# Kernel optimization log

Measured on AMD Instinct MI355X. Metric: run time of the kernel, lower is better.

The kernel has to match this reference:

```python
import math
import jax, jax.numpy as jnp
import numpy as np

EMBED_DIM = 1024
NUM_HEADS = 16
HEAD_DIM = EMBED_DIM // NUM_HEADS
B, S = 4, 2048


def setup_inputs() -> dict:
    key = jax.random.key(0)
    ks = jax.random.split(key, 12)
    sc = 1.0 / math.sqrt(EMBED_DIM)
    inp = {
        "query": jax.random.normal(ks[0], (B, S, EMBED_DIM), jnp.float32),
        "key": jax.random.normal(ks[1], (B, S, EMBED_DIM), jnp.float32),
        "value": jax.random.normal(ks[2], (B, S, EMBED_DIM), jnp.float32),
        # causal mask: True = masked (upper triangle above diagonal)
        "attn_mask": jnp.triu(jnp.ones((S, S), jnp.bool_), k=1),
        "q_w": jax.random.normal(ks[3], (EMBED_DIM, EMBED_DIM), jnp.float32) * sc,
        "q_b": jax.random.normal(ks[4], (EMBED_DIM,), jnp.float32) * sc,
        "k_w": jax.random.normal(ks[5], (EMBED_DIM, EMBED_DIM), jnp.float32) * sc,
        "k_b": jax.random.normal(ks[6], (EMBED_DIM,), jnp.float32) * sc,
        "v_w": jax.random.normal(ks[7], (EMBED_DIM, EMBED_DIM), jnp.float32) * sc,
        "v_b": jax.random.normal(ks[8], (EMBED_DIM,), jnp.float32) * sc,
        "o_w": jax.random.normal(ks[9], (EMBED_DIM, EMBED_DIM), jnp.float32) * sc,
        "o_b": jax.random.normal(ks[10], (EMBED_DIM,), jnp.float32) * sc,
    }
    return inp


def _split_heads(x):
    # (B, S, E) -> (B, H, S, D)
    b, s, _ = x.shape
    return x.reshape(b, s, NUM_HEADS, HEAD_DIM).transpose(0, 2, 1, 3)


def reference(query, key, value, attn_mask, q_w, q_b, k_w, k_b, v_w, v_b, o_w, o_b):
    # torch Linear: y = x @ W.T + b
    q = _split_heads(query @ q_w.T + q_b)
    k = _split_heads(key @ k_w.T + k_b)
    v = _split_heads(value @ v_w.T + v_b)
    scale = math.sqrt(HEAD_DIM)
    scores = jnp.einsum("bhqd,bhkd->bhqk", q, k) / scale
    scores = jnp.where(attn_mask[None, None, :, :], -jnp.inf, scores)
    attn = jax.nn.softmax(scores, axis=-1)
    ctx = jnp.einsum("bhqk,bhkd->bhqd", attn, v)  # (B,H,S,D)
    ctx = ctx.transpose(0, 2, 1, 3).reshape(query.shape[0], query.shape[1], EMBED_DIM)
    return ctx @ o_w.T + o_b
```

## Files before the change

kernel.cpp:

```cpp
#include <hip/hip_runtime.h>
#include <stdint.h>

#define BB 4
#define SS 2048
#define EE 1024
#define HH 16
#define DD 64
#define MM (BB*SS)

typedef unsigned short u16;
typedef __attribute__((ext_vector_type(8))) short bf16x8;
typedef __attribute__((ext_vector_type(4))) float f32x4;

#define MFMA __builtin_amdgcn_mfma_f32_16x16x32_bf16

__device__ __forceinline__ u16 f2bf(float f) {
  union { float f; uint32_t u; } x; x.f = f;
  uint32_t r = (x.u + 0x7fffu + ((x.u >> 16) & 1u)) >> 16;
  return (u16)r;
}

__device__ __forceinline__ uint32_t cvtpk(float lo, float hi) {
  uint32_t r;
  asm volatile("v_cvt_pk_bf16_f32 %0, %1, %2" : "=v"(r) : "v"(lo), "v"(hi));
  return r;
}

__device__ __forceinline__ void gl_lds16(const void* g, void* l) {
  __builtin_amdgcn_global_load_lds(
      (const __attribute__((address_space(1))) uint32_t*)g,
      (__attribute__((address_space(3))) uint32_t*)l, 16, 0, 0);
}

__global__ __launch_bounds__(256) void cast_all(
    const float* __restrict__ a0, const float* __restrict__ a1,
    const float* __restrict__ a2,
    const float* __restrict__ w0, const float* __restrict__ w1,
    const float* __restrict__ w2, const float* __restrict__ w3,
    u16* __restrict__ da0, u16* __restrict__ da1, u16* __restrict__ da2,
    u16* __restrict__ dw0, u16* __restrict__ dw1,
    u16* __restrict__ dw2, u16* __restrict__ dw3) {
  int i = blockIdx.x * 256 + threadIdx.x;
  const float* s; u16* d; int off;
  if (i < 3 * (1 << 20)) {
    int sel = i >> 20; off = i & ((1 << 20) - 1);
    s = sel == 0 ? a0 : sel == 1 ? a1 : a2;
    d = sel == 0 ? da0 : sel == 1 ? da1 : da2;
  } else {
    int k = i - 3 * (1 << 20);
    int sel = k >> 17; off = k & ((1 << 17) - 1);
    s = sel == 0 ? w0 : sel == 1 ? w1 : sel == 2 ? w2 : w3;
    d = sel == 0 ? dw0 : sel == 1 ? dw1 : sel == 2 ? dw2 : dw3;
  }
  const float4* sp = (const float4*)s;
  float4 a = sp[off*2], b = sp[off*2+1];
  union { u16 h[8]; uint4 v; } o;
  o.h[0]=f2bf(a.x); o.h[1]=f2bf(a.y); o.h[2]=f2bf(a.z); o.h[3]=f2bf(a.w);
  o.h[4]=f2bf(b.x); o.h[5]=f2bf(b.y); o.h[6]=f2bf(b.z); o.h[7]=f2bf(b.w);
  *(uint4*)(d + (size_t)off*8) = o.v;
}

template<int OUT_BF16>
__device__ __forceinline__ void gemm_body(
    const u16* __restrict__ A, const u16* __restrict__ W,
    const float* __restrict__ bias, void* __restrict__ Cout,
    int Ndim, int Kdim, float scale, int m0, int n0,
    u16* As, u16* Bs) {
  const int tid = threadIdx.x;
  const int lane = tid & 63, w = tid >> 6;
  const int wr = w >> 1, wc = w & 1;
  const int srow = tid >> 2;
  const int scol = (tid & 3) * 8;

  f32x4 acc[4][4] = {};

  const u16* ag = A + (size_t)(m0 + srow) * Kdim + scol;
  const u16* bg = W + (size_t)(n0 + srow) * Kdim + scol;
  const size_t rstride = (size_t)64 * Kdim;
  const int l15 = lane & 15;
  const int fke = (lane >> 4) * 8;

  for (int k0 = 0; k0 < Kdim; k0 += 32) {
    gl_lds16(ag + k0,           As + tid*8);
    gl_lds16(ag + k0 + rstride, As + 2048 + tid*8);
    gl_lds16(bg + k0,           Bs + tid*8);
    gl_lds16(bg + k0 + rstride, Bs + 2048 + tid*8);
    __syncthreads();

    bf16x8 af[4], bfr[4];
    #pragma unroll
    for (int m = 0; m < 4; ++m)
      af[m] = *(const bf16x8*)(As + (wr*64 + m*16 + l15)*32 + fke);
    #pragma unroll
    for (int n = 0; n < 4; ++n)
      bfr[n] = *(const bf16x8*)(Bs + (wc*64 + n*16 + l15)*32 + fke);
    #pragma unroll
    for (int m = 0; m < 4; ++m)
      #pragma unroll
      for (int n = 0; n < 4; ++n)
        acc[m][n] = MFMA(af[m], bfr[n], acc[m][n], 0, 0, 0);
    __syncthreads();
  }

  const int ccol = wc*64 + l15;
  float bv[4];
  #pragma unroll
  for (int n = 0; n < 4; ++n) bv[n] = bias[n0 + ccol + n*16];
  #pragma unroll
  for (int m = 0; m < 4; ++m) {
    #pragma unroll
    for (int i = 0; i < 4; ++i) {
      size_t row = (size_t)(m0 + wr*64 + m*16 + (lane>>4)*4 + i);
      #pragma unroll
      for (int n = 0; n < 4; ++n) {
        float v = (acc[m][n][i] + bv[n]) * scale;
        size_t idx = row * Ndim + (n0 + ccol + n*16);
        if (OUT_BF16) ((u16*)Cout)[idx] = f2bf(v);
        else          ((float*)Cout)[idx] = v;
      }
    }
  }
}

__global__ __launch_bounds__(256, 2) void gemm_qkv(
    const u16* __restrict__ qx, const u16* __restrict__ kx, const u16* __restrict__ vx,
    const u16* __restrict__ wqm, const u16* __restrict__ wkm, const u16* __restrict__ wvm,
    const float* __restrict__ qbv, const float* __restrict__ kbv, const float* __restrict__ vbv,
    u16* __restrict__ qo, u16* __restrict__ ko, u16* __restrict__ vo) {
  __shared__ alignas(16) u16 As[128*32];
  __shared__ alignas(16) u16 Bs[128*32];
  const int flat = blockIdx.x + blockIdx.y * 8 + blockIdx.z * 512;
  const int j = flat & 7, s = flat >> 3;
  const int c = 3*j + (s >> 6), i = s & 63;
  const int nx = i & 7, yy = ((c & 7) << 3) + (i >> 3);
  const int z = c >> 3;
  const u16* A = z == 0 ? qx : z == 1 ? kx : vx;
  const u16* W = z == 0 ? wqm : z == 1 ? wkm : wvm;
  const float* bias = z == 0 ? qbv : z == 1 ? kbv : vbv;
  u16* C = z == 0 ? qo : z == 1 ? ko : vo;
  const float scale = z == 0 ? 0.125f : 1.0f;
  gemm_body<1>(A, W, bias, C, EE, EE, scale, yy * 128, nx * 128, As, Bs);
}

__global__ __launch_bounds__(256, 2) void gemm_out(
    const u16* __restrict__ A, const u16* __restrict__ W,
    const float* __restrict__ bias, float* __restrict__ Cout) {
  __shared__ alignas(16) u16 As[128*32];
  __shared__ alignas(16) u16 Bs[128*32];
  const int flat = blockIdx.x + blockIdx.y * 8;
  const int j = flat & 7, s = flat >> 3;
  const int nx = s & 7, yy = (j << 3) + (s >> 3);
  gemm_body<0>(A, W, bias, Cout, EE, EE, 1.0f, yy * 128, nx * 128, As, Bs);
}

__global__ __launch_bounds__(256, 2) void attn8(
    const u16* __restrict__ Q, const u16* __restrict__ K,
    const u16* __restrict__ V, u16* __restrict__ ctx) {
  __shared__ alignas(16) u16 Ks[2][64*64];
  __shared__ alignas(16) u16 VTs[2][64*64];
  __shared__ alignas(16) u16 Ps[4][32*64];

  const int tid = threadIdx.x, lane = tid & 63, w = tid >> 6;
  const int l15 = lane & 15, l4 = lane >> 4;

  const int f = blockIdx.x;
  const int j = f & 7, s = f >> 3;
  const int qlo = s & 7;
  const int panel = j * 8 + (s >> 3);
  const int h = panel & 15, b = panel >> 4;
  const size_t base = ((size_t)b * SS) * EE + h * DD;

  const int kr  = tid >> 3;
  const int ksl = tid & 7;
  const int rv  = tid >> 2;
  const int vc  = tid & 3;

  u16* KsE  = (u16*)Ks;
  u16* VTsE = (u16*)VTs;
  u16* PsE  = (u16*)Ps + w * 2048;

  auto stageK = [&](int t, int bi) {
    #pragma unroll
    for (int i = 0; i < 2; ++i) {
      int row = i*32 + kr;
      gl_lds16(K + base + (size_t)(t*64 + row)*EE + (ksl ^ (row & 7))*8,
               KsE + bi*4096 + i*2048 + tid*8);
    }
  };
  auto vtWrite = [&](int bi, bf16x8 v0, bf16x8 v1) {
    #pragma unroll
    for (int jj = 0; jj < 16; ++jj) {
      u16 val = jj < 8 ? (u16)v0[jj] : (u16)v1[jj - 8];
      int d = vc*16 + jj;
      int sl = (rv >> 3) ^ (jj & 7) ^ (vc << 1);
      VTsE[bi*4096 + d*64 + sl*8 + (rv & 7)] = val;
    }
  };

  #pragma unroll 1
  for (int pass = 0; pass < 2; ++pass) {
    const int qblk = pass == 0 ? (15 - qlo) : qlo;
    const int q0 = qblk * 128, wq = q0 + w * 32;
    const int ntile = 2 * qblk + 2;

    bf16x8 qf[2][2];
    #pragma unroll
    for (int G = 0; G < 2; ++G)
      #pragma unroll
      for (int kc = 0; kc < 2; ++kc)
        qf[G][kc] = *(const bf16x8*)(Q + base + (size_t)(wq + G*16 + l15)*EE + kc*32 + l4*8);

    f32x4 o[2][4] = {};
    float lsum[2] = {0.f, 0.f};

    {
      const u16* vs = V + base + (size_t)rv*EE + vc*16;
      bf16x8 v0 = *(const bf16x8*)vs;
      bf16x8 v1 = *(const bf16x8*)(vs + 8);
      stageK(0, 0);
      vtWrite(0, v0, v1);
    }
    __syncthreads();

    for (int t = 0; t < ntile; ++t) {
      const int cur = t & 1;
      const bool havenext = (t + 1 < ntile);
      bf16x8 nv0, nv1;
      if (havenext) {
        const u16* vs = V + base + (size_t)((t+1)*64 + rv)*EE + vc*16;
        nv0 = *(const bf16x8*)vs;
        nv1 = *(const bf16x8*)(vs + 8);
        stageK(t + 1, cur ^ 1);
      }

      const bool active = (wq + 31 >= t*64);
      const bool g0act  = (wq + 15 >= t*64);
      if (active) {
        f32x4 sc[2][4] = {};
        #pragma unroll
        for (int nt = 0; nt < 4; ++nt) {
          int row = nt*16 + l15;
          int sw = row & 7;
          const u16* kb = KsE + cur*4096 + row*64;
          bf16x8 kf0 = *(const bf16x8*)(kb + ((l4    ) ^ sw)*8);
          bf16x8 kf1 = *(const bf16x8*)(kb + ((4 + l4) ^ sw)*8);
          sc[1][nt] = MFMA(kf0, qf[1][0], sc[1][nt], 0, 0, 0);
          sc[1][nt] = MFMA(kf1, qf[1][1], sc[1][nt], 0, 0, 0);
          if (g0act) {
            sc[0][nt] = MFMA(kf0, qf[0][0], sc[0][nt], 0, 0, 0);
            sc[0][nt] = MFMA(kf1, qf[0][1], sc[0][nt], 0, 0, 0);
          }
        }

        #pragma unroll
        for (int G = 0; G < 2; ++G) {
          if (G == 0 && !g0act) continue;
          const bool nomask = (t*64 + 63 <= wq + G*16);
          const int qg = wq + G*16 + l15;
          #pragma unroll
          for (int nt = 0; nt < 4; ++nt) {
            float p0 = exp2f(__builtin_fmaf(sc[G][nt][0], 1.44269504f, -17.3123405f));
            float p1 = exp2f(__builtin_fmaf(sc[G][nt][1], 1.44269504f, -17.3123405f));
            float p2 = exp2f(__builtin_fmaf(sc[G][nt][2], 1.44269504f, -17.3123405f));
            float p3 = exp2f(__builtin_fmaf(sc[G][nt][3], 1.44269504f, -17.3123405f));
            if (!nomask) {
              int kvs = t*64 + nt*16 + l4*4;
              if (kvs + 0 > qg) p0 = 0.f;
              if (kvs + 1 > qg) p1 = 0.f;
              if (kvs + 2 > qg) p2 = 0.f;
              if (kvs + 3 > qg) p3 = 0.f;
            }
            lsum[G] += (p0 + p1) + (p2 + p3);
            uint2 pk;
            pk.x = cvtpk(p0, p1);
            pk.y = cvtpk(p2, p3);
            *(uint2*)((char*)PsE + (G*16 + l15)*128
                          + (((nt*2 + (l4 >> 1)) ^ (l15 & 7)) * 16)
                          + (l4 & 1) * 8) = pk;
          }
        }
      }

      if (havenext) vtWrite(cur ^ 1, nv0, nv1);

      if (active) {
        #pragma unroll
        for (int cc = 0; cc < 2; ++cc) {
          bf16x8 pf1 = *(const bf16x8*)((char*)PsE + (16 + l15)*128
                                       + (((cc*4 + l4) ^ (l15 & 7)) * 16));
          bf16x8 pf0;
          if (g0act)
            pf0 = *(const bf16x8*)((char*)PsE + l15*128
                                       + (((cc*4 + l4) ^ (l15 & 7)) * 16));
          #pragma unroll
          for (int dm = 0; dm < 4; ++dm) {
            int sl = (cc*4 + l4) ^ (l15 & 7) ^ (dm << 1);
            bf16x8 vfv = *(const bf16x8*)(VTsE + cur*4096 + (dm*16 + l15)*64 + sl*8);
            o[1][dm] = MFMA(pf1, vfv, o[1][dm], 0, 0, 0);
            if (g0act) o[0][dm] = MFMA(pf0, vfv, o[0][dm], 0, 0, 0);
          }
        }
      }
      __syncthreads();
    }

    #pragma unroll
    for (int G = 0; G < 2; ++G) {
      float r = lsum[G];
      r += __shfl_xor(r, 16);
      r += __shfl_xor(r, 32);
      lsum[G] = 1.0f / r;
    }

    #pragma unroll
    for (int G = 0; G < 2; ++G)
      #pragma unroll
      for (int i = 0; i < 4; ++i) {
        float invv = __shfl(lsum[G], l4*4 + i);
        size_t roff = base + (size_t)(wq + G*16 + l4*4 + i) * EE;
        #pragma unroll
        for (int dm = 0; dm < 4; ++dm)
          ctx[roff + dm*16 + l15] = f2bf(o[G][dm][i] * invv);
      }
  }
}

extern "C" void kernel_launch(void* const* d_in, const int* in_sizes, int n_in,
                              void* d_out, int out_size, void* d_ws, size_t ws_size,
                              hipStream_t stream) {
  const float* query = (const float*)d_in[0];
  const float* key   = (const float*)d_in[1];
  const float* value = (const float*)d_in[2];
  const float* q_w = (const float*)d_in[4];
  const float* q_b = (const float*)d_in[5];
  const float* k_w = (const float*)d_in[6];
  const float* k_b = (const float*)d_in[7];
  const float* v_w = (const float*)d_in[8];
  const float* v_b = (const float*)d_in[9];
  const float* o_w = (const float*)d_in[10];
  const float* o_b = (const float*)d_in[11];

  char* ws = (char*)d_ws;
  const size_t XB = (size_t)MM * EE * 2;
  const size_t WB = (size_t)EE * EE * 2;
  u16* qx = (u16*)(ws);
  u16* kx = (u16*)(ws + XB);
  u16* vx = (u16*)(ws + 2*XB);
  u16* wq = (u16*)(ws + 3*XB);
  u16* wk = (u16*)(ws + 3*XB + WB);
  u16* wv = (u16*)(ws + 3*XB + 2*WB);
  u16* wo = (u16*)(ws + 3*XB + 3*WB);
  u16* qp = (u16*)(ws + 3*XB + 4*WB);
  u16* kp = (u16*)(ws + 4*XB + 4*WB);
  u16* vp = (u16*)(ws + 5*XB + 4*WB);
  u16* ctxb = qx;

  const int ncast = 3 * (1 << 20) + 4 * (1 << 17);
  cast_all<<<ncast/256, 256, 0, stream>>>(query, key, value,
                                          q_w, k_w, v_w, o_w,
                                          qx, kx, vx, wq, wk, wv, wo);

  gemm_qkv<<<dim3(EE/128, MM/128, 3), 256, 0, stream>>>(
      qx, kx, vx, wq, wk, wv, q_b, k_b, v_b, qp, kp, vp);

  attn8<<<512, 256, 0, stream>>>(qp, kp, vp, ctxb);

  gemm_out<<<dim3(EE/128, MM/128), 256, 0, stream>>>(ctxb, wo, o_b, (float*)d_out);
}
```

Before: 197.9 us.

## Process KV tiles in pairs per barrier and use native exp2

The attention kernel now stages two 64-row K/V tiles per pipeline step, doubling the LDS buffers. It processes both tiles between a single __syncthreads, which halves the barrier count and gives global loads more time to land. It also swaps exp2f for the hardware exp2 builtin when available. In exchange, LDS use grows from about 48KB to 80KB per block, which may cut occupancy below two blocks per CU, and more V registers are live across the step.

New measurement: 183.9 us. 7.1% less time.

```diff
diff --git a/kernel.cpp b/kernel.cpp
--- a/kernel.cpp
+++ b/kernel.cpp
@@ -13,6 +13,12 @@
 typedef __attribute__((ext_vector_type(4))) float f32x4;
 
 #define MFMA __builtin_amdgcn_mfma_f32_16x16x32_bf16
+
+#if __has_builtin(__builtin_amdgcn_exp2f)
+#define EXP2(x) __builtin_amdgcn_exp2f(x)
+#else
+#define EXP2(x) exp2f(x)
+#endif
 
 __device__ __forceinline__ u16 f2bf(float f) {
   union { float f; uint32_t u; } x; x.f = f;
@@ -153,11 +159,11 @@
   gemm_body<0>(A, W, bias, Cout, EE, EE, 1.0f, yy * 128, nx * 128, As, Bs);
 }
 
-__global__ __launch_bounds__(256, 2) void attn8(
+__global__ __launch_bounds__(256, 2) void attn9(
     const u16* __restrict__ Q, const u16* __restrict__ K,
     const u16* __restrict__ V, u16* __restrict__ ctx) {
-  __shared__ alignas(16) u16 Ks[2][64*64];
-  __shared__ alignas(16) u16 VTs[2][64*64];
+  __shared__ alignas(16) u16 Ks[2][2][64*64];
+  __shared__ alignas(16) u16 VTs[2][2][64*64];
   __shared__ alignas(16) u16 Ps[4][32*64];
 
   const int tid = threadIdx.x, lane = tid & 63, w = tid >> 6;
@@ -179,21 +185,21 @@
   u16* VTsE = (u16*)VTs;
   u16* PsE  = (u16*)Ps + w * 2048;
 
-  auto stageK = [&](int t, int bi) {
+  auto stageK = [&](int t, int pb, int sub) {
     #pragma unroll
     for (int i = 0; i < 2; ++i) {
       int row = i*32 + kr;
       gl_lds16(K + base + (size_t)(t*64 + row)*EE + (ksl ^ (row & 7))*8,
-               KsE + bi*4096 + i*2048 + tid*8);
+               KsE + pb*8192 + sub*4096 + i*2048 + tid*8);
     }
   };
-  auto vtWrite = [&](int bi, bf16x8 v0, bf16x8 v1) {
+  auto vtWrite = [&](int pb, int sub, bf16x8 v0, bf16x8 v1) {
     #pragma unroll
     for (int jj = 0; jj < 16; ++jj) {
       u16 val = jj < 8 ? (u16)v0[jj] : (u16)v1[jj - 8];
       int d = vc*16 + jj;
       int sl = (rv >> 3) ^ (jj & 7) ^ (vc << 1);
-      VTsE[bi*4096 + d*64 + sl*8 + (rv & 7)] = val;
+      VTsE[pb*8192 + sub*4096 + d*64 + sl*8 + (rv & 7)] = val;
     }
   };
 
@@ -201,7 +207,7 @@
   for (int pass = 0; pass < 2; ++pass) {
     const int qblk = pass == 0 ? (15 - qlo) : qlo;
     const int q0 = qblk * 128, wq = q0 + w * 32;
-    const int ntile = 2 * qblk + 2;
+    const int npairs = qblk + 1;
 
     bf16x8 qf[2][2];
     #pragma unroll
@@ -213,94 +219,103 @@
     f32x4 o[2][4] = {};
     float lsum[2] = {0.f, 0.f};
 
-    {
-      const u16* vs = V + base + (size_t)rv*EE + vc*16;
-      bf16x8 v0 = *(const bf16x8*)vs;
-      bf16x8 v1 = *(const bf16x8*)(vs + 8);
-      stageK(0, 0);
-      vtWrite(0, v0, v1);
-    }
-    __syncthreads();
-
-    for (int t = 0; t < ntile; ++t) {
-      const int cur = t & 1;
-      const bool havenext = (t + 1 < ntile);
-      bf16x8 nv0, nv1;
-      if (havenext) {
-        const u16* vs = V + base + (size_t)((t+1)*64 + rv)*EE + vc*16;
-        nv0 = *(const bf16x8*)vs;
-        nv1 = *(const bf16x8*)(vs + 8);
-        stageK(t + 1, cur ^ 1);
-      }
-
-      const bool active = (wq + 31 >= t*64);
-      const bool g0act  = (wq + 15 >= t*64);
-      if (active) {
-        f32x4 sc[2][4] = {};
+    auto computeTile = [&](int t, int pb, int sub) {
+      if (wq + 31 < t*64) return;
+      const bool g0act = (wq + 15 >= t*64);
+      const u16* tileK = KsE + pb*8192 + sub*4096;
+      const u16* tileV = VTsE + pb*8192 + sub*4096;
+
+      f32x4 sc[2][4] = {};
+      #pragma unroll
+      for (int nt = 0; nt < 4; ++nt) {
+        int row = nt*16 + l15;
+        int sw = row & 7;
+        const u16* kb = tileK + row*64;
+        bf16x8 kf0 = *(const bf16x8*)(kb + ((l4    ) ^ sw)*8);
+        bf16x8 kf1 = *(const bf16x8*)(kb + ((4 + l4) ^ sw)*8);
+        sc[1][nt] = MFMA(kf0, qf[1][0], sc[1][nt], 0, 0, 0);
+        sc[1][nt] = MFMA(kf1, qf[1][1], sc[1][nt], 0, 0, 0);
+        if (g0act) {
+          sc[0][nt] = MFMA(kf0, qf[0][0], sc[0][nt], 0, 0, 0);
+          sc[0][nt] = MFMA(kf1, qf[0][1], sc[0][nt], 0, 0, 0);
+        }
+      }
+
+      #pragma unroll
+      for (int G = 0; G < 2; ++G) {
+        if (G == 0 && !g0act) continue;
+        const bool nomask = (t*64 + 63 <= wq + G*16);
+        const int qg = wq + G*16 + l15;
         #pragma unroll
         for (int nt = 0; nt < 4; ++nt) {
-          int row = nt*16 + l15;
-          int sw = row & 7;
-          const u16* kb = KsE + cur*4096 + row*64;
-          bf16x8 kf0 = *(const bf16x8*)(kb + ((l4    ) ^ sw)*8);
-          bf16x8 kf1 = *(const bf16x8*)(kb + ((4 + l4) ^ sw)*8);
-          sc[1][nt] = MFMA(kf0, qf[1][0], sc[1][nt], 0, 0, 0);
-          sc[1][nt] = MFMA(kf1, qf[1][1], sc[1][nt], 0, 0, 0);
-          if (g0act) {
-            sc[0][nt] = MFMA(kf0, qf[0][0], sc[0][nt], 0, 0, 0);
-            sc[0][nt] = MFMA(kf1, qf[0][1], sc[0][nt], 0, 0, 0);
+          float p0 = EXP2(__builtin_fmaf(sc[G][nt][0], 1.44269504f, -17.3123405f));
+          float p1 = EXP2(__builtin_fmaf(sc[G][nt][1], 1.44269504f, -17.3123405f));
+          float p2 = EXP2(__builtin_fmaf(sc[G][nt][2], 1.44269504f, -17.3123405f));
+          float p3 = EXP2(__builtin_fmaf(sc[G][nt][3], 1.44269504f, -17.3123405f));
+          if (!nomask) {
+            int kvs = t*64 + nt*16 + l4*4;
+            if (kvs + 0 > qg) p0 = 0.f;
+            if (kvs + 1 > qg) p1 = 0.f;
+            if (kvs + 2 > qg) p2 = 0.f;
+            if (kvs + 3 > qg) p3 = 0.f;
           }
+          lsum[G] += (p0 + p1) + (p2 + p3);
+          uint2 pk;
+          pk.x = cvtpk(p0, p1);
+          pk.y = cvtpk(p2, p3);
+          *(uint2*)((char*)PsE + (G*16 + l15)*128
+                        + (((nt*2 + (l4 >> 1)) ^ (l15 & 7)) * 16)
+                        + (l4 & 1) * 8) = pk;
         }
-
+      }
+
+      #pragma unroll
+      for (int cc = 0; cc < 2; ++cc) {
+        bf16x8 pf1 = *(const bf16x8*)((char*)PsE + (16 + l15)*128
+                                     + (((cc*4 + l4) ^ (l15 & 7)) * 16));
+        bf16x8 pf0;
+        if (g0act)
+          pf0 = *(const bf16x8*)((char*)PsE + l15*128
+                                     + (((cc*4 + l4) ^ (l15 & 7)) * 16));
         #pragma unroll
-        for (int G = 0; G < 2; ++G) {
-          if (G == 0 && !g0act) continue;
-          const bool nomask = (t*64 + 63 <= wq + G*16);
-          const int qg = wq + G*16 + l15;
-          #pragma unroll
-          for (int nt = 0; nt < 4; ++nt) {
-            float p0 = exp2f(__builtin_fmaf(sc[G][nt][0], 1.44269504f, -17.3123405f));
-            float p1 = exp2f(__builtin_fmaf(sc[G][nt][1], 1.44269504f, -17.3123405f));
-            float p2 = exp2f(__builtin_fmaf(sc[G][nt][2], 1.44269504f, -17.3123405f));
-            float p3 = exp2f(__builtin_fmaf(sc[G][nt][3], 1.44269504f, -17.3123405f));
-            if (!nomask) {
-              int kvs = t*64 + nt*16 + l4*4;
-              if (kvs + 0 > qg) p0 = 0.f;
-              if (kvs + 1 > qg) p1 = 0.f;
-              if (kvs + 2 > qg) p2 = 0.f;
-              if (kvs + 3 > qg) p3 = 0.f;
-            }
-            lsum[G] += (p0 + p1) + (p2 + p3);
-            uint2 pk;
-            pk.x = cvtpk(p0, p1);
-            pk.y = cvtpk(p2, p3);
-            *(uint2*)((char*)PsE + (G*16 + l15)*128
-                          + (((nt*2 + (l4 >> 1)) ^ (l15 & 7)) * 16)
-                          + (l4 & 1) * 8) = pk;
-          }
+        for (int dm = 0; dm < 4; ++dm) {
+          int sl = (cc*4 + l4) ^ (l15 & 7) ^ (dm << 1);
+          bf16x8 vfv = *(const bf16x8*)(tileV + (dm*16 + l15)*64 + sl*8);
+          o[1][dm] = MFMA(pf1, vfv, o[1][dm], 0, 0, 0);
+          if (g0act) o[0][dm] = MFMA(pf0, vfv, o[0][dm], 0, 0, 0);
         }
       }
-
-      if (havenext) vtWrite(cur ^ 1, nv0, nv1);
-
-      if (active) {
-        #pragma unroll
-        for (int cc = 0; cc < 2; ++cc) {
-          bf16x8 pf1 = *(const bf16x8*)((char*)PsE + (16 + l15)*128
-                                       + (((cc*4 + l4) ^ (l15 & 7)) * 16));
-          bf16x8 pf0;
-          if (g0act)
-            pf0 = *(const bf16x8*)((char*)PsE + l15*128
-                                       + (((cc*4 + l4) ^ (l15 & 7)) * 16));
-          #pragma unroll
-          for (int dm = 0; dm < 4; ++dm) {
-            int sl = (cc*4 + l4) ^ (l15 & 7) ^ (dm << 1);
-            bf16x8 vfv = *(const bf16x8*)(VTsE + cur*4096 + (dm*16 + l15)*64 + sl*8);
-            o[1][dm] = MFMA(pf1, vfv, o[1][dm], 0, 0, 0);
-            if (g0act) o[0][dm] = MFMA(pf0, vfv, o[0][dm], 0, 0, 0);
-          }
-        }
-      }
+    };
+
+    {
+      const u16* va = V + base + (size_t)rv*EE + vc*16;
+      const u16* vb = V + base + (size_t)(64 + rv)*EE + vc*16;
+      bf16x8 a0 = *(const bf16x8*)va, a1 = *(const bf16x8*)(va + 8);
+      bf16x8 b0 = *(const bf16x8*)vb, b1 = *(const bf16x8*)(vb + 8);
+      stageK(0, 0, 0);
+      stageK(1, 0, 1);
+      vtWrite(0, 0, a0, a1);
+      vtWrite(0, 1, b0, b1);
+    }
+    __syncthreads();
+
+    for (int u = 0; u < npairs; ++u) {
+      const int cur = u & 1;
+      const bool havenext = (u + 1 < npairs);
+      bf16x8 na0, na1, nb0, nb1;
+      if (havenext) {
+        const u16* va = V + base + (size_t)((2*u+2)*64 + rv)*EE + vc*16;
+        const u16* vb = V + base + (size_t)((2*u+3)*64 + rv)*EE + vc*16;
+        na0 = *(const bf16x8*)va; na1 = *(const bf16x8*)(va + 8);
+        nb0 = *(const bf16x8*)vb; nb1 = *(const bf16x8*)(vb + 8);
+        stageK(2*u+2, cur ^ 1, 0);
+        stageK(2*u+3, cur ^ 1, 1);
+      }
+
+      computeTile(2*u, cur, 0);
+      if (havenext) vtWrite(cur ^ 1, 0, na0, na1);
+      computeTile(2*u + 1, cur, 1);
+      if (havenext) vtWrite(cur ^ 1, 1, nb0, nb1);
       __syncthreads();
     }
 
@@ -363,7 +378,7 @@
   gemm_qkv<<<dim3(EE/128, MM/128, 3), 256, 0, stream>>>(
       qx, kx, vx, wq, wk, wv, q_b, k_b, v_b, qp, kp, vp);
 
-  attn8<<<512, 256, 0, stream>>>(qp, kp, vp, ctxb);
+  attn9<<<512, 256, 0, stream>>>(qp, kp, vp, ctxb);
 
   gemm_out<<<dim3(EE/128, MM/128), 256, 0, stream>>>(ctxb, wo, o_b, (float*)d_out);
 }
```
